# Optimization experiments

Measured on AMD Instinct MI355X. Metric: run time of the kernel, lower is better.

## Reference

```python
import jax, jax.numpy as jnp
import numpy as np

HID, HEADS = 1024, 16
HEAD_DIM = HID // HEADS

def _rope_table(seq_len, d):
    inv_freq = 1.0 / (10000.0 ** (jnp.arange(0, d, 2, dtype=jnp.float32) / d))  # [d/2]
    sin_inp = jnp.arange(seq_len, dtype=jnp.float32)[:, None] * inv_freq[None, :]  # [S, d/2]
    return jnp.concatenate([jnp.sin(sin_inp), jnp.cos(sin_inp)], axis=-1)  # [S, d]

def _apply_rope(x, pos_emb):
    # Faithful to original: cos/sin of the (already sin/cos) pos_emb values.
    half = x.shape[-1] // 2
    x1, x2 = x[..., :half], x[..., half:]
    p1, p2 = pos_emb[..., :half], pos_emb[..., half:]
    return jnp.concatenate([x1 * jnp.cos(p1) + x2 * jnp.sin(p1),
                            x2 * jnp.cos(p2) - x1 * jnp.sin(p2)], axis=-1)

def setup_inputs() -> dict:
    key = jax.random.key(0)
    ks = jax.random.split(key, 11)
    B, S = 8, 1024
    s = 1.0 / np.sqrt(HID)
    return {
        'query': jax.random.normal(ks[0], (B, S, HID), jnp.float32),
        'key':   jax.random.normal(ks[1], (B, S, HID), jnp.float32),
        'value': jax.random.normal(ks[2], (B, S, HID), jnp.float32),
        'Wq': jax.random.normal(ks[3], (HID, HID), jnp.float32) * s,
        'bq': jax.random.normal(ks[4], (HID,), jnp.float32) * s,
        'Wk': jax.random.normal(ks[5], (HID, HID), jnp.float32) * s,
        'bk': jax.random.normal(ks[6], (HID,), jnp.float32) * s,
        'Wv': jax.random.normal(ks[7], (HID, HID), jnp.float32) * s,
        'bv': jax.random.normal(ks[8], (HID,), jnp.float32) * s,
        'Wo': jax.random.normal(ks[9], (HID, HID), jnp.float32) * s,
        'bo': jax.random.normal(ks[10], (HID,), jnp.float32) * s,
    }

def reference(query, key, value, Wq, bq, Wk, bk, Wv, bv, Wo, bo):
    B, S, _ = query.shape
    q = query @ Wq.T + bq
    k = key @ Wk.T + bk
    v = value @ Wv.T + bv
    pos_emb = _rope_table(S, HID)
    q = _apply_rope(q, pos_emb)
    k = _apply_rope(k, pos_emb)
    v = _apply_rope(v, pos_emb)  # original applies RoPE to V too
    # split heads: [B, H, S, D]
    q = q.reshape(B, S, HEADS, HEAD_DIM).transpose(0, 2, 1, 3)
    k = k.reshape(B, S, HEADS, HEAD_DIM).transpose(0, 2, 1, 3)
    v = v.reshape(B, S, HEADS, HEAD_DIM).transpose(0, 2, 1, 3)
    scale = jnp.sqrt(jnp.float32(HEAD_DIM))
    attn = jnp.einsum('bhqd,bhkd->bhqk', q, k) / scale
    attn = jax.nn.softmax(attn, axis=-1)  # dropout=0.0 (eval): identity
    x = jnp.einsum('bhqk,bhkd->bhqd', attn, v)
    x = x.transpose(0, 2, 1, 3).reshape(B, S, HID)
    return x @ Wo.T + bo
```

## Files before the change

### kernel.cpp

```cpp
#include <hip/hip_runtime.h>
#include <hip/hip_fp16.h>
#include <cmath>


typedef _Float16 f16;
typedef __attribute__((ext_vector_type(4))) _Float16 f16x4;
typedef __attribute__((ext_vector_type(8))) _Float16 f16x8;
typedef __attribute__((ext_vector_type(4))) float f32x4;

#define MFMA16(a, b, c) __builtin_amdgcn_mfma_f32_16x16x32_f16((a), (b), (c), 0, 0, 0)
#define MFMA16K16(a, b, c) __builtin_amdgcn_mfma_f32_16x16x16f16((a), (b), (c), 0, 0, 0)

__device__ __forceinline__ void g2l16(void* lds, const void* g) {
  __builtin_amdgcn_global_load_lds(
      (const __attribute__((address_space(1))) void*)g,
      (__attribute__((address_space(3))) void*)lds,
      16, 0, 0);
}

__global__ void cvt3_kernel(const float* __restrict__ a, const float* __restrict__ b,
                            const float* __restrict__ c,
                            f16* __restrict__ oa, f16* __restrict__ ob, f16* __restrict__ oc) {
  const float* src;
  f16* dst;
  if (blockIdx.y == 0) { src = a; dst = oa; }
  else if (blockIdx.y == 1) { src = b; dst = ob; }
  else { src = c; dst = oc; }
  size_t t = (size_t)blockIdx.x * 256 + threadIdx.x;
  float4 v = ((const float4*)src)[t];
  f16x4 w = { (f16)v.x, (f16)v.y, (f16)v.z, (f16)v.w };
  ((f16x4*)dst)[t] = w;
}

__global__ void cvt4_kernel(const float* __restrict__ a, const float* __restrict__ b,
                            const float* __restrict__ c, const float* __restrict__ d,
                            f16* __restrict__ oa, f16* __restrict__ ob,
                            f16* __restrict__ oc, f16* __restrict__ od) {
  const float* src;
  f16* dst;
  if (blockIdx.y == 0) { src = a; dst = oa; }
  else if (blockIdx.y == 1) { src = b; dst = ob; }
  else if (blockIdx.y == 2) { src = c; dst = oc; }
  else { src = d; dst = od; }
  size_t t = (size_t)blockIdx.x * 256 + threadIdx.x;
  float4 v = ((const float4*)src)[t];
  f16x4 w = { (f16)v.x, (f16)v.y, (f16)v.z, (f16)v.w };
  ((f16x4*)dst)[t] = w;
}

struct GemmBatch {
  const f16* A[3];
  const f16* W[3];
  const float* bias[3];
  void* O[3];
  float scale[3];
};

template <bool OUT_F16>
__global__ __launch_bounds__(256)
void gemm_f16_kernel(GemmBatch gb) {
  __shared__ __align__(16) f16 sA[128 * 64];
  __shared__ __align__(16) f16 sB[128 * 64];
  const int z = blockIdx.z;
  const f16* __restrict__ A = gb.A[z];
  const f16* __restrict__ Bw = gb.W[z];
  const float* __restrict__ bias = gb.bias[z];
  void* __restrict__ Out = gb.O[z];
  const float sc = gb.scale[z];

  const int tid = threadIdx.x;
  const int lane = tid & 63;
  const int wv = tid >> 6;
  const int l15 = lane & 15;
  const int quad = lane >> 4;

  const int flat = blockIdx.x + (blockIdx.y << 3);
  const int xcd = flat & 7;
  const int t64 = flat >> 3;
  const int m0 = (xcd * 8 + (t64 & 7)) * 128;
  const int n0 = (t64 >> 3) * 128;

  const int wm = (wv & 1) * 64;
  const int wn = (wv >> 1) * 64;

  const int srow = lane >> 3;
  const int schunk = (lane & 7) ^ srow;
  const f16* gA = A + (size_t)(m0 + wv * 32 + srow) * 1024 + schunk * 8;
  const f16* gB = Bw + (size_t)(n0 + wv * 32 + srow) * 1024 + schunk * 8;
  f16* lA = sA + (wv * 32) * 64;
  f16* lB = sB + (wv * 32) * 64;

  f32x4 acc[4][4] = {};

  for (int k0 = 0; k0 < 1024; k0 += 64) {
    __syncthreads();
#pragma unroll
    for (int j = 0; j < 4; ++j) {
      g2l16(lA + j * 8 * 64, gA + (size_t)j * 8 * 1024 + k0);
      g2l16(lB + j * 8 * 64, gB + (size_t)j * 8 * 1024 + k0);
    }
    __syncthreads();
#pragma unroll
    for (int kc = 0; kc < 2; ++kc) {
      f16x8 af[4], bf[4];
#pragma unroll
      for (int t = 0; t < 4; ++t) {
        const int swz = ((kc * 4 + quad) ^ (l15 & 7)) * 8;
        af[t] = *(const f16x8*)(sA + (wm + t * 16 + l15) * 64 + swz);
        bf[t] = *(const f16x8*)(sB + (wn + t * 16 + l15) * 64 + swz);
      }
#pragma unroll
      for (int mi = 0; mi < 4; ++mi)
#pragma unroll
        for (int ni = 0; ni < 4; ++ni)
          acc[mi][ni] = MFMA16(af[mi], bf[ni], acc[mi][ni]);
    }
  }

#pragma unroll
  for (int ni = 0; ni < 4; ++ni) {
    const int col = n0 + wn + ni * 16 + l15;
    const float bv = bias[col];
#pragma unroll
    for (int mi = 0; mi < 4; ++mi) {
      const int row0 = m0 + wm + mi * 16 + quad * 4;
#pragma unroll
      for (int r = 0; r < 4; ++r) {
        float v = (acc[mi][ni][r] + bv) * sc;
        if (OUT_F16)
          ((f16*)Out)[(size_t)(row0 + r) * 1024 + col] = (f16)v;
        else
          ((float*)Out)[(size_t)(row0 + r) * 1024 + col] = v;
      }
    }
  }
}

__global__ __launch_bounds__(256)
void rope_kernel(f16* __restrict__ q, f16* __restrict__ k,
                 const f16* __restrict__ v, f16* __restrict__ vt) {
  __shared__ f16 sT[128 * 72];
  const int t = threadIdx.x;
  const int c0 = blockIdx.x * 64;
  const int s0 = blockIdx.y * 64;
  const int b = blockIdx.z;
  const int sr = t >> 2;
  const int cq = (t & 3) * 16;
  const int s = s0 + sr;

  float c1[16], s1[16], c2[16], s2[16];
#pragma unroll
  for (int j = 0; j < 16; ++j) {
    const int i = c0 + cq + j;
    const float invf = exp2f((float)i * -0.025952563241307517f);
    const float th = (float)s * invf;
    const float p1 = sinf(th), p2 = cosf(th);
    c1[j] = __cosf(p1); s1[j] = __sinf(p1);
    c2[j] = __cosf(p2); s2[j] = __sinf(p2);
  }

  const size_t base = ((size_t)(b * 1024 + s)) * 1024 + c0 + cq;

#pragma unroll
  for (int tz = 0; tz < 2; ++tz) {
    f16* ptr = tz ? k : q;
    f16x8 x1a = *(f16x8*)(ptr + base);
    f16x8 x1b = *(f16x8*)(ptr + base + 8);
    f16x8 x2a = *(f16x8*)(ptr + base + 512);
    f16x8 x2b = *(f16x8*)(ptr + base + 520);
    f16x8 r1a, r1b, r2a, r2b;
#pragma unroll
    for (int j = 0; j < 8; ++j) {
      float a0 = (float)x1a[j], b0 = (float)x2a[j];
      float a1 = (float)x1b[j], b1 = (float)x2b[j];
      r1a[j] = (f16)(a0 * c1[j] + b0 * s1[j]);
      r2a[j] = (f16)(b0 * c2[j] - a0 * s2[j]);
      r1b[j] = (f16)(a1 * c1[8 + j] + b1 * s1[8 + j]);
      r2b[j] = (f16)(b1 * c2[8 + j] - a1 * s2[8 + j]);
    }
    *(f16x8*)(ptr + base) = r1a;
    *(f16x8*)(ptr + base + 8) = r1b;
    *(f16x8*)(ptr + base + 512) = r2a;
    *(f16x8*)(ptr + base + 520) = r2b;
  }

  {
    f16x8 x1a = *(const f16x8*)(v + base);
    f16x8 x1b = *(const f16x8*)(v + base + 8);
    f16x8 x2a = *(const f16x8*)(v + base + 512);
    f16x8 x2b = *(const f16x8*)(v + base + 520);
#pragma unroll
    for (int j = 0; j < 8; ++j) {
      float a0 = (float)x1a[j], b0 = (float)x2a[j];
      float a1 = (float)x1b[j], b1 = (float)x2b[j];
      sT[(cq + j) * 72 + sr] = (f16)(a0 * c1[j] + b0 * s1[j]);
      sT[(64 + cq + j) * 72 + sr] = (f16)(b0 * c2[j] - a0 * s2[j]);
      sT[(cq + 8 + j) * 72 + sr] = (f16)(a1 * c1[8 + j] + b1 * s1[8 + j]);
      sT[(64 + cq + 8 + j) * 72 + sr] = (f16)(b1 * c2[8 + j] - a1 * s2[8 + j]);
    }
  }
  __syncthreads();

  const int lr = t >> 1;
  const int sh = (t & 1) * 32;
  const int h = (lr < 64) ? (c0 >> 6) : (8 + (c0 >> 6));
  const int d = lr & 63;
  const size_t gbase = ((size_t)((b * 16 + h) * 64 + d)) * 1024 + s0 + sh;
#pragma unroll
  for (int m = 0; m < 4; ++m)
    *(f16x8*)(vt + gbase + m * 8) = *(const f16x8*)(sT + lr * 72 + sh + m * 8);
}

__global__ __launch_bounds__(512, 4)
void attn_kernel(const f16* __restrict__ q, const f16* __restrict__ k,
                 const f16* __restrict__ vt, f16* __restrict__ xo) {
  __shared__ __align__(16) f16 smem[32768];
  const int tid = threadIdx.x;
  const int lane = tid & 63;
  const int wv = tid >> 6;
  const int l15 = lane & 15;
  const int quad = lane >> 4;
  const int bh = blockIdx.x;
  const int qt = blockIdx.y;
  const int b = bh >> 4, h = bh & 15;
  const size_t hidbase = ((size_t)b << 20) + (size_t)(h << 6);
  const int sq0 = qt * 128 + wv * 16;

  f16x8 fq[2];
#pragma unroll
  for (int kc = 0; kc < 2; ++kc)
    fq[kc] = *(const f16x8*)(q + hidbase + (size_t)(sq0 + l15) * 1024 + kc * 32 + quad * 8);

  f32x4 ot[4] = {};
  f32x4 ls = {};
  const f16x4 fone = { (f16)1.0f, (f16)1.0f, (f16)1.0f, (f16)1.0f };

  const int srowK = lane >> 3;
  const int schunkK = (lane & 7) ^ srowK;
  const f16* gK = k + hidbase + (size_t)(wv * 16 + srowK) * 1024 + schunkK * 8;
  const int vrow = lane >> 4;
  const f16* gVbase = vt + ((size_t)bh * 64) * 1024;

  auto STAGE = [&](int kt, int bf) {
    f16* sK = smem + bf * 16384;
    f16* sV = sK + 8192;
    const int sk0 = kt * 128;
#pragma unroll
    for (int j = 0; j < 2; ++j)
      g2l16(sK + (wv * 16 + j * 8) * 64, gK + (size_t)(sk0 + j * 8) * 1024);
#pragma unroll
    for (int i = 0; i < 2; ++i) {
      const int row = wv * 8 + i * 4 + vrow;
      const int gch = (lane & 15) ^ (row & 15);
      g2l16(sV + (wv * 8 + i * 4) * 128, gVbase + (size_t)row * 1024 + sk0 + gch * 8);
    }
  };

  STAGE(0, 0);

  for (int kt = 0; kt < 8; ++kt) {
    const int cur = kt & 1;
    __builtin_amdgcn_sched_barrier(0);
    __builtin_amdgcn_s_barrier();
    __builtin_amdgcn_sched_barrier(0);
    if (kt < 7) {
      STAGE(kt + 1, cur ^ 1);
      asm volatile("s_waitcnt vmcnt(4)" ::: "memory");
    } else {
      asm volatile("s_waitcnt vmcnt(0)" ::: "memory");
    }
    __builtin_amdgcn_sched_barrier(0);
    __builtin_amdgcn_s_barrier();
    __builtin_amdgcn_sched_barrier(0);

    const f16* sK = smem + cur * 16384;
    const f16* sV = sK + 8192;

#pragma unroll
    for (int nj = 0; nj < 8; ++nj) {
      f32x4 st = { -12.0f, -12.0f, -12.0f, -12.0f };
#pragma unroll
      for (int kc = 0; kc < 2; ++kc) {
        f16x8 fk = *(const f16x8*)(sK + (nj * 16 + l15) * 64 +
                                   ((kc * 4 + quad) ^ (l15 & 7)) * 8);
        st = MFMA16(fk, fq[kc], st);
      }
      const float p0 = exp2f(st[0]);
      const float p1 = exp2f(st[1]);
      const float p2 = exp2f(st[2]);
      const float p3 = exp2f(st[3]);
      auto plo = __builtin_amdgcn_cvt_pkrtz(p0, p1);
      auto phi = __builtin_amdgcn_cvt_pkrtz(p2, p3);
      f16x4 pf;
      pf[0] = (f16)plo[0]; pf[1] = (f16)plo[1];
      pf[2] = (f16)phi[0]; pf[3] = (f16)phi[1];
      ls = MFMA16K16(fone, pf, ls);
#pragma unroll
      for (int nd = 0; nd < 4; ++nd) {
        f16x4 fv = *(const f16x4*)(sV + (nd * 16 + l15) * 128 +
                                   ((nj * 2 + (quad >> 1)) ^ l15) * 8 + (quad & 1) * 4);
        ot[nd] = MFMA16K16(fv, pf, ot[nd]);
      }
    }
  }

  const float inv = 1.0f / ls[0];

  f16* sO = smem + wv * (16 * 72);
#pragma unroll
  for (int nd = 0; nd < 4; ++nd) {
    f16x4 w;
#pragma unroll
    for (int r = 0; r < 4; ++r) w[r] = (f16)(ot[nd][r] * inv);
    *(f16x4*)(sO + l15 * 72 + nd * 16 + quad * 4) = w;
  }
  const int orow = lane >> 2;
  const int oseg = (lane & 3) * 16;
  const size_t gb = hidbase + (size_t)(sq0 + orow) * 1024 + oseg;
  *(f16x8*)(xo + gb) = *(const f16x8*)(sO + orow * 72 + oseg);
  *(f16x8*)(xo + gb + 8) = *(const f16x8*)(sO + orow * 72 + oseg + 8);
}

extern "C" void kernel_launch(void* const* d_in, const int* in_sizes, int n_in,
                              void* d_out, int out_size, void* d_ws, size_t ws_size,
                              hipStream_t stream) {
  const float* query = (const float*)d_in[0];
  const float* key   = (const float*)d_in[1];
  const float* value = (const float*)d_in[2];
  const float* Wq = (const float*)d_in[3];
  const float* bq = (const float*)d_in[4];
  const float* Wk = (const float*)d_in[5];
  const float* bk = (const float*)d_in[6];
  const float* Wv = (const float*)d_in[7];
  const float* bv = (const float*)d_in[8];
  const float* Wo = (const float*)d_in[9];
  const float* bo = (const float*)d_in[10];

  char* ws = (char*)d_ws;
  const size_t SZT = (size_t)8 * 1024 * 1024 * 2;
  const size_t SZW = (size_t)1024 * 1024 * 2;
  f16* Xq  = (f16*)(ws);
  f16* Xk  = (f16*)(ws + SZT);
  f16* Xv  = (f16*)(ws + 2 * SZT);
  f16* Wqh = (f16*)(ws + 3 * SZT);
  f16* Wkh = (f16*)(ws + 3 * SZT + SZW);
  f16* Wvh = (f16*)(ws + 3 * SZT + 2 * SZW);
  f16* Woh = (f16*)(ws + 3 * SZT + 3 * SZW);
  f16* Qp  = (f16*)(ws + 3 * SZT + 4 * SZW);
  f16* Kp  = (f16*)(ws + 4 * SZT + 4 * SZW);
  f16* Vp  = (f16*)(ws + 5 * SZT + 4 * SZW);
  f16* Vt  = (f16*)(ws + 6 * SZT + 4 * SZW);
  f16* Xat = (f16*)(ws + 7 * SZT + 4 * SZW);

  cvt3_kernel<<<dim3(8192, 3), 256, 0, stream>>>(query, key, value, Xq, Xk, Xv);
  cvt4_kernel<<<dim3(1024, 4), 256, 0, stream>>>(Wq, Wk, Wv, Wo, Wqh, Wkh, Wvh, Woh);

  const float SCQ = 0.18033688011112042f;
  GemmBatch gqkv;
  gqkv.A[0] = Xq;  gqkv.A[1] = Xk;  gqkv.A[2] = Xv;
  gqkv.W[0] = Wqh; gqkv.W[1] = Wkh; gqkv.W[2] = Wvh;
  gqkv.bias[0] = bq; gqkv.bias[1] = bk; gqkv.bias[2] = bv;
  gqkv.O[0] = Qp;  gqkv.O[1] = Kp;  gqkv.O[2] = Vp;
  gqkv.scale[0] = SCQ; gqkv.scale[1] = 1.0f; gqkv.scale[2] = 1.0f;
  gemm_f16_kernel<true><<<dim3(8, 64, 3), 256, 0, stream>>>(gqkv);

  rope_kernel<<<dim3(8, 16, 8), 256, 0, stream>>>(Qp, Kp, Vp, Vt);

  attn_kernel<<<dim3(128, 8), 512, 0, stream>>>(Qp, Kp, Vt, Xat);

  GemmBatch go;
  go.A[0] = Xat; go.A[1] = nullptr; go.A[2] = nullptr;
  go.W[0] = Woh; go.W[1] = nullptr; go.W[2] = nullptr;
  go.bias[0] = bo; go.bias[1] = nullptr; go.bias[2] = nullptr;
  go.O[0] = d_out; go.O[1] = nullptr; go.O[2] = nullptr;
  go.scale[0] = 1.0f; go.scale[1] = 1.0f; go.scale[2] = 1.0f;
  gemm_f16_kernel<false><<<dim3(8, 64, 1), 256, 0, stream>>>(go);
}
```

Measured before the change: 323.6 us.

## Double-buffer GEMM LDS tiles to overlap global loads with MFMA compute

```diff
diff --git a/kernel.cpp b/kernel.cpp
--- a/kernel.cpp
+++ b/kernel.cpp
@@ -59,8 +59,8 @@
 template <bool OUT_F16>
 __global__ __launch_bounds__(256)
 void gemm_f16_kernel(GemmBatch gb) {
-  __shared__ __align__(16) f16 sA[128 * 64];
-  __shared__ __align__(16) f16 sB[128 * 64];
+  __shared__ __align__(16) f16 sA[2][128 * 64];
+  __shared__ __align__(16) f16 sB[2][128 * 64];
   const int z = blockIdx.z;
   const f16* __restrict__ A = gb.A[z];
   const f16* __restrict__ Bw = gb.W[z];
@@ -87,27 +87,42 @@
   const int schunk = (lane & 7) ^ srow;
   const f16* gA = A + (size_t)(m0 + wv * 32 + srow) * 1024 + schunk * 8;
   const f16* gB = Bw + (size_t)(n0 + wv * 32 + srow) * 1024 + schunk * 8;
-  f16* lA = sA + (wv * 32) * 64;
-  f16* lB = sB + (wv * 32) * 64;
 
   f32x4 acc[4][4] = {};
 
-  for (int k0 = 0; k0 < 1024; k0 += 64) {
-    __syncthreads();
+  auto STAGE = [&](int t, int bi) {
 #pragma unroll
     for (int j = 0; j < 4; ++j) {
-      g2l16(lA + j * 8 * 64, gA + (size_t)j * 8 * 1024 + k0);
-      g2l16(lB + j * 8 * 64, gB + (size_t)j * 8 * 1024 + k0);
-    }
-    __syncthreads();
+      g2l16(&sA[bi][(wv * 32 + j * 8) * 64], gA + (size_t)j * 8 * 1024 + t * 64);
+      g2l16(&sB[bi][(wv * 32 + j * 8) * 64], gB + (size_t)j * 8 * 1024 + t * 64);
+    }
+  };
+
+  STAGE(0, 0);
+
+  for (int t = 0; t < 16; ++t) {
+    const int cur = t & 1;
+    __builtin_amdgcn_sched_barrier(0);
+    __builtin_amdgcn_s_barrier();
+    __builtin_amdgcn_sched_barrier(0);
+    if (t < 15) {
+      STAGE(t + 1, cur ^ 1);
+      asm volatile("s_waitcnt vmcnt(8)" ::: "memory");
+    } else {
+      asm volatile("s_waitcnt vmcnt(0)" ::: "memory");
+    }
+    __builtin_amdgcn_sched_barrier(0);
+    __builtin_amdgcn_s_barrier();
+    __builtin_amdgcn_sched_barrier(0);
+
 #pragma unroll
     for (int kc = 0; kc < 2; ++kc) {
       f16x8 af[4], bf[4];
 #pragma unroll
-      for (int t = 0; t < 4; ++t) {
+      for (int t4 = 0; t4 < 4; ++t4) {
         const int swz = ((kc * 4 + quad) ^ (l15 & 7)) * 8;
-        af[t] = *(const f16x8*)(sA + (wm + t * 16 + l15) * 64 + swz);
-        bf[t] = *(const f16x8*)(sB + (wn + t * 16 + l15) * 64 + swz);
+        af[t4] = *(const f16x8*)(&sA[cur][(wm + t4 * 16 + l15) * 64 + swz]);
+        bf[t4] = *(const f16x8*)(&sB[cur][(wn + t4 * 16 + l15) * 64 + swz]);
       }
 #pragma unroll
       for (int mi = 0; mi < 4; ++mi)
```

New measurement: 325.4 us. Within noise of the previous version (+0.6%).
